# Optimization experiments

Measured on AMD Instinct MI355X. Metric: run time of the kernel, lower is better.

Reference implementation:

```python
import jax, jax.numpy as jnp
import numpy as np

B, T, D = 2, 2048, 1024
N, H = 16, 64  # num_heads, head_dim


def setup_inputs() -> dict:
    key = jax.random.key(0)
    ks = jax.random.split(key, 8)
    glorot = lambda k, shape, fan_in, fan_out: jax.random.uniform(
        k, shape, jnp.float32, -1.0, 1.0) * np.sqrt(6.0 / (fan_in + fan_out))
    return {
        "q": jax.random.normal(ks[0], (B, T, D), jnp.float32),
        "v": jax.random.normal(ks[1], (B, T, D), jnp.float32),
        "k": jax.random.normal(ks[2], (B, T, D), jnp.float32),
        "w_query": glorot(ks[3], (D, N, H), D, N * H),
        "b_query": jnp.zeros((N, 1, H), jnp.float32),
        "w_value": glorot(ks[4], (D, N, H), D, N * H),
        "b_value": jnp.zeros((N, 1, H), jnp.float32),
        "w_key": glorot(ks[5], (D, N, H), D, N * H),
        "b_key": jnp.zeros((N, 1, H), jnp.float32),
        "w_projection": glorot(ks[6], (N, D, H), N * H, D),
        "b_projection": jnp.zeros((1, D), jnp.float32),
    }


def reference(q, v, k, w_query, b_query, w_value, b_value, w_key, b_key,
              w_projection, b_projection):
    # QKV projections: [B,T,D] x [D,N,H] -> [B,N,T,H]
    query = jnp.einsum('btd,dnh->bnth', q, w_query) + b_query
    value = jnp.einsum('btd,dnh->bnth', v, w_value) + b_value
    key_p = jnp.einsum('btd,dnh->bnth', k, w_key) + b_key
    # Scaled dot-product attention, scores divided by sqrt(head_dim)
    scale = 1.0 / jnp.sqrt(jnp.asarray(H, query.dtype))
    scores = jnp.einsum('bnth,bnsh->bnts', query, key_p) * scale  # [B,N,T,T]
    weights = jax.nn.softmax(scores, axis=-1)
    attn = jnp.einsum('bnts,bnsh->bnth', weights, value)
    # Output projection: [B,N,T,H] x [N,D,H] -> [B,T,D]
    out = jnp.einsum('bnth,ndh->btd', attn, w_projection) + b_projection
    return out
```

## Files before the change

kernel.cpp:

```cpp
#include <hip/hip_runtime.h>
#include <hip/hip_bf16.h>
#include <cstdint>
#include <cstddef>


typedef __attribute__((ext_vector_type(8))) short short8;
typedef __attribute__((ext_vector_type(4))) float floatx4;
typedef __attribute__((ext_vector_type(8))) unsigned short ushort8;

#define EXP2F(x) __builtin_amdgcn_exp2f(x)

static __device__ __forceinline__ unsigned short f2bf(float f) {
    union { float f; unsigned int u; } v; v.f = f;
    unsigned int r = v.u + 0x7fffu + ((v.u >> 16) & 1u);
    return (unsigned short)(r >> 16);
}
static __device__ __forceinline__ unsigned int pk2bf(float lo, float hi) {
    __hip_bfloat162 t = __float22bfloat162_rn(make_float2(lo, hi));
    union { __hip_bfloat162 h; unsigned int u; } c; c.h = t;
    return c.u;
}
static __device__ __forceinline__ void gl_lds16(const unsigned short* g, unsigned short* l) {
    __builtin_amdgcn_global_load_lds(
        (const __attribute__((address_space(1))) unsigned int*)g,
        (__attribute__((address_space(3))) unsigned int*)l, 16, 0, 0);
}

__global__ __launch_bounds__(256) void mha_transpose_w(
    const float* __restrict__ wq, const float* __restrict__ wk, const float* __restrict__ wv,
    unsigned short* __restrict__ wqT, unsigned short* __restrict__ wkT, unsigned short* __restrict__ wvT)
{
    __shared__ float tile[32][33];
    const float* src; unsigned short* dst;
    int z = blockIdx.z;
    if (z == 0)      { src = wq; dst = wqT; }
    else if (z == 1) { src = wk; dst = wkT; }
    else             { src = wv; dst = wvT; }
    int n0 = blockIdx.x * 32, d0 = blockIdx.y * 32;
    int tx = threadIdx.x, ty = threadIdx.y;
    #pragma unroll
    for (int j = 0; j < 4; ++j)
        tile[ty + j * 8][tx] = src[(size_t)(d0 + ty + j * 8) * 1024 + n0 + tx];
    __syncthreads();
    #pragma unroll
    for (int j = 0; j < 4; ++j)
        dst[(size_t)(n0 + ty + j * 8) * 1024 + d0 + tx] = f2bf(tile[tx][ty + j * 8]);
}

__global__ __launch_bounds__(256) void mha_reorder_wp(
    const float* __restrict__ wp, unsigned short* __restrict__ wp2)
{
    int base = blockIdx.x * 1024 + threadIdx.x;
    #pragma unroll
    for (int i = 0; i < 4; ++i) {
        int idx = base + i * 256;
        int n = idx >> 16, d = (idx >> 6) & 1023, h = idx & 63;
        wp2[(size_t)d * 1024 + n * 64 + h] = f2bf(wp[idx]);
    }
}

__global__ __launch_bounds__(256) void prep_bf16_3(
    const float* __restrict__ x0, const float* __restrict__ x1, const float* __restrict__ x2,
    unsigned short* __restrict__ o0, unsigned short* __restrict__ o1, unsigned short* __restrict__ o2)
{
    int y = blockIdx.y;
    const float* x = y == 0 ? x0 : (y == 1 ? x1 : x2);
    unsigned short* o = y == 0 ? o0 : (y == 1 ? o1 : o2);
    size_t i = ((size_t)blockIdx.x * 256 + threadIdx.x) * 8;
    float4 a = *(const float4*)(x + i);
    float4 b = *(const float4*)(x + i + 4);
    uint4 pk;
    pk.x = pk2bf(a.x, a.y); pk.y = pk2bf(a.z, a.w);
    pk.z = pk2bf(b.x, b.y); pk.w = pk2bf(b.z, b.w);
    *(uint4*)(o + i) = pk;
}

__global__ __launch_bounds__(256) void gemm_qkv128(
    const unsigned short* __restrict__ A0, const unsigned short* __restrict__ A1,
    const unsigned short* __restrict__ A2,
    const unsigned short* __restrict__ W0, const unsigned short* __restrict__ W1,
    const unsigned short* __restrict__ W2,
    const float* __restrict__ b0, const float* __restrict__ b1, const float* __restrict__ b2,
    unsigned short* __restrict__ O0, unsigned short* __restrict__ O1, unsigned short* __restrict__ O2,
    float qscale, int matSel)
{
    __shared__ unsigned short As[128 * 32];
    __shared__ unsigned short Bs[128 * 32];
    int bm = blockIdx.x, by = blockIdx.y;
    int mat, nt;
    if (matSel < 0) { mat = by >> 3; nt = by & 7; } else { mat = matSel; nt = by; }
    const unsigned short* A  = mat == 0 ? A0 : (mat == 1 ? A1 : A2);
    const unsigned short* WT = mat == 0 ? W0 : (mat == 1 ? W1 : W2);
    const float* bias        = mat == 0 ? b0 : (mat == 1 ? b1 : b2);
    unsigned short* Out      = mat == 0 ? O0 : (mat == 1 ? O1 : O2);
    float scale = (mat == 0) ? qscale : 1.0f;
    int vmode = (mat == 2);

    int tid = threadIdx.x;
    int w = tid >> 6, lane = tid & 63, c15 = lane & 15, quad = lane >> 4;
    int wm = w >> 1, wn = w & 1;

    const unsigned short* gA[2]; unsigned short* lA[2];
    const unsigned short* gB[2]; unsigned short* lB[2];
    #pragma unroll
    for (int i = 0; i < 2; ++i) {
        int s = (w * 2 + i) * 64 + lane;
        gA[i] = A  + (size_t)(bm * 128 + (s >> 2)) * 1024 + (s & 3) * 8;
        lA[i] = &As[s * 8];
        gB[i] = WT + (size_t)(nt * 128 + (s >> 2)) * 1024 + (s & 3) * 8;
        lB[i] = &Bs[s * 8];
    }

    floatx4 acc[4][4];
    #pragma unroll
    for (int mi = 0; mi < 4; ++mi)
        #pragma unroll
        for (int ni = 0; ni < 4; ++ni) acc[mi][ni] = (floatx4){0.f, 0.f, 0.f, 0.f};

    for (int kt = 0; kt < 32; ++kt) {
        __syncthreads();
        #pragma unroll
        for (int i = 0; i < 2; ++i) { gl_lds16(gA[i] + kt * 32, lA[i]); gl_lds16(gB[i] + kt * 32, lB[i]); }
        __syncthreads();
        short8 af[4], bfr[4];
        #pragma unroll
        for (int mi = 0; mi < 4; ++mi)
            af[mi] = *(const short8*)&As[(wm * 64 + mi * 16 + c15) * 32 + quad * 8];
        #pragma unroll
        for (int ni = 0; ni < 4; ++ni)
            bfr[ni] = *(const short8*)&Bs[(wn * 64 + ni * 16 + c15) * 32 + quad * 8];
        #pragma unroll
        for (int mi = 0; mi < 4; ++mi)
            #pragma unroll
            for (int ni = 0; ni < 4; ++ni)
                acc[mi][ni] = __builtin_amdgcn_mfma_f32_16x16x32_bf16(af[mi], bfr[ni], acc[mi][ni], 0, 0, 0);
    }
    #pragma unroll
    for (int mi = 0; mi < 4; ++mi)
        #pragma unroll
        for (int ni = 0; ni < 4; ++ni)
            #pragma unroll
            for (int r = 0; r < 4; ++r) {
                int row = bm * 128 + wm * 64 + mi * 16 + quad * 4 + r;
                int col = nt * 128 + wn * 64 + ni * 16 + c15;
                float val = (acc[mi][ni][r] + bias[col]) * scale;
                int b = row >> 11, t = row & 2047, n = col >> 6, h = col & 63;
                if (vmode)
                    Out[((size_t)(b * 16 + n) * 64 + h) * 2048 + t] = f2bf(val);
                else
                    Out[((size_t)(b * 16 + n) * 2048 + t) * 64 + h] = f2bf(val);
            }
}

__global__ __launch_bounds__(256) void mha_flash3(
    const unsigned short* __restrict__ Qp, const unsigned short* __restrict__ Kp,
    const unsigned short* __restrict__ Vt, unsigned short* __restrict__ attnb)
{
    __shared__ unsigned short Ks[64 * 72];
    __shared__ unsigned short Vs[64 * 72];
    __shared__ unsigned short Pl[4][32 * 72];

    int bi = blockIdx.x;
    int xcd = bi & 7, j = bi >> 3;
    int bn = xcd * 4 + (j >> 4), qt = j & 15;
    int b = bn >> 4, n = bn & 15;
    int tid = threadIdx.x;
    int w = tid >> 6, lane = tid & 63, c15 = lane & 15, quad = lane >> 4;

    const unsigned short* Qb = Qp + (size_t)bn * 2048 * 64;
    const unsigned short* Kb = Kp + (size_t)bn * 2048 * 64;
    const unsigned short* Vb = Vt + (size_t)bn * 64 * 2048;

    int qbase = qt * 128 + w * 32;

    short8 bQ[2][2];
    #pragma unroll
    for (int tni = 0; tni < 2; ++tni)
        #pragma unroll
        for (int kc = 0; kc < 2; ++kc)
            bQ[tni][kc] = *(const short8*)(Qb + (size_t)(qbase + tni * 16 + c15) * 64 + kc * 32 + quad * 8);

    float l_i[2] = {0.f, 0.f};
    floatx4 o[2][4];
    #pragma unroll
    for (int i = 0; i < 2; ++i)
        #pragma unroll
        for (int j2 = 0; j2 < 4; ++j2) o[i][j2] = (floatx4){0.f, 0.f, 0.f, 0.f};

    unsigned short* Pw = &Pl[w][0];
    int srow = tid >> 3, scc = tid & 7;

    ushort8 kreg[2], vreg[2];
    #pragma unroll
    for (int i = 0; i < 2; ++i) {
        kreg[i] = *(const ushort8*)(Kb + (size_t)(srow + i * 32) * 64 + scc * 8);
        vreg[i] = *(const ushort8*)(Vb + (size_t)(srow + i * 32) * 2048 + scc * 8);
    }

    for (int it = 0; it < 32; ++it) {
        __syncthreads();
        #pragma unroll
        for (int i = 0; i < 2; ++i) {
            *(ushort8*)&Ks[(srow + i * 32) * 72 + scc * 8] = kreg[i];
            *(ushort8*)&Vs[(srow + i * 32) * 72 + scc * 8] = vreg[i];
        }
        if (it < 31) {
            int s1 = (it + 1) * 64;
            #pragma unroll
            for (int i = 0; i < 2; ++i) {
                kreg[i] = *(const ushort8*)(Kb + (size_t)(s1 + srow + i * 32) * 64 + scc * 8);
                vreg[i] = *(const ushort8*)(Vb + (size_t)(srow + i * 32) * 2048 + s1 + scc * 8);
            }
        }
        __syncthreads();

        floatx4 sc[4][2];
        #pragma unroll
        for (int smi = 0; smi < 4; ++smi) {
            short8 a0 = *(const short8*)&Ks[(smi * 16 + c15) * 72 + quad * 8];
            short8 a1 = *(const short8*)&Ks[(smi * 16 + c15) * 72 + 32 + quad * 8];
            #pragma unroll
            for (int tni = 0; tni < 2; ++tni) {
                floatx4 t = (floatx4){0.f, 0.f, 0.f, 0.f};
                t = __builtin_amdgcn_mfma_f32_16x16x32_bf16(a0, bQ[tni][0], t, 0, 0, 0);
                t = __builtin_amdgcn_mfma_f32_16x16x32_bf16(a1, bQ[tni][1], t, 0, 0, 0);
                sc[smi][tni] = t;
            }
        }
        #pragma unroll
        for (int tni = 0; tni < 2; ++tni) {
            float rs = 0.f;
            #pragma unroll
            for (int smi = 0; smi < 4; ++smi) {
                float p0 = EXP2F(sc[smi][tni][0]);
                float p1 = EXP2F(sc[smi][tni][1]);
                float p2 = EXP2F(sc[smi][tni][2]);
                float p3 = EXP2F(sc[smi][tni][3]);
                rs += (p0 + p1) + (p2 + p3);
                uint2 pw;
                pw.x = pk2bf(p0, p1);
                pw.y = pk2bf(p2, p3);
                *(uint2*)&Pw[(tni * 16 + c15) * 72 + smi * 16 + quad * 4] = pw;
            }
            l_i[tni] += rs;
        }
        short8 bv[4][2];
        #pragma unroll
        for (int hni = 0; hni < 4; ++hni)
            #pragma unroll
            for (int kc = 0; kc < 2; ++kc)
                bv[hni][kc] = *(const short8*)&Vs[(hni * 16 + c15) * 72 + kc * 32 + quad * 8];
        #pragma unroll
        for (int tmi = 0; tmi < 2; ++tmi) {
            short8 ap0 = *(const short8*)&Pw[(tmi * 16 + c15) * 72 + quad * 8];
            short8 ap1 = *(const short8*)&Pw[(tmi * 16 + c15) * 72 + 32 + quad * 8];
            #pragma unroll
            for (int hni = 0; hni < 4; ++hni) {
                o[tmi][hni] = __builtin_amdgcn_mfma_f32_16x16x32_bf16(ap0, bv[hni][0], o[tmi][hni], 0, 0, 0);
                o[tmi][hni] = __builtin_amdgcn_mfma_f32_16x16x32_bf16(ap1, bv[hni][1], o[tmi][hni], 0, 0, 0);
            }
        }
    }
    float lf[2];
    #pragma unroll
    for (int tmi = 0; tmi < 2; ++tmi) {
        float s = l_i[tmi];
        s += __shfl_xor(s, 16, 64);
        s += __shfl_xor(s, 32, 64);
        lf[tmi] = s;
    }
    #pragma unroll
    for (int tmi = 0; tmi < 2; ++tmi)
        #pragma unroll
        for (int r = 0; r < 4; ++r) {
            float linv = 1.0f / __shfl(lf[tmi], quad * 4 + r, 64);
            int t = qbase + tmi * 16 + quad * 4 + r;
            #pragma unroll
            for (int hni = 0; hni < 4; ++hni) {
                int col = n * 64 + hni * 16 + c15;
                attnb[(size_t)(b * 2048 + t) * 1024 + col] = f2bf(o[tmi][hni][r] * linv);
            }
        }
}

__global__ __launch_bounds__(256) void gemm_out64v2(
    const unsigned short* __restrict__ A, const unsigned short* __restrict__ BT,
    const float* __restrict__ bias, float* __restrict__ out)
{
    __shared__ unsigned short As[64 * 64];
    __shared__ unsigned short Bs[128 * 64];
    int bm = blockIdx.x, nt = blockIdx.y;
    int tid = threadIdx.x;
    int w = tid >> 6, lane = tid & 63, c15 = lane & 15, quad = lane >> 4;
    int wm = w >> 1, wn = w & 1;

    const unsigned short* gA[2]; unsigned short* lA[2];
    const unsigned short* gB[4]; unsigned short* lB[4];
    #pragma unroll
    for (int i = 0; i < 2; ++i) {
        int s = (w * 2 + i) * 64 + lane;
        int row = s >> 3, cl = (s & 7) ^ (row & 7);
        gA[i] = A + (size_t)(bm * 64 + row) * 1024 + cl * 8;
        lA[i] = &As[s * 8];
    }
    #pragma unroll
    for (int i = 0; i < 4; ++i) {
        int s = (w * 4 + i) * 64 + lane;
        int row = s >> 3, cl = (s & 7) ^ (row & 7);
        gB[i] = BT + (size_t)(nt * 128 + row) * 1024 + cl * 8;
        lB[i] = &Bs[s * 8];
    }

    floatx4 acc[2][4];
    #pragma unroll
    for (int mi = 0; mi < 2; ++mi)
        #pragma unroll
        for (int ni = 0; ni < 4; ++ni) acc[mi][ni] = (floatx4){0.f, 0.f, 0.f, 0.f};

    for (int kt = 0; kt < 16; ++kt) {
        __syncthreads();
        #pragma unroll
        for (int i = 0; i < 2; ++i) gl_lds16(gA[i] + kt * 64, lA[i]);
        #pragma unroll
        for (int i = 0; i < 4; ++i) gl_lds16(gB[i] + kt * 64, lB[i]);
        __syncthreads();
        #pragma unroll
        for (int kc = 0; kc < 2; ++kc) {
            short8 af[2], bfr[4];
            #pragma unroll
            for (int mi = 0; mi < 2; ++mi) {
                int row = wm * 32 + mi * 16 + c15;
                af[mi] = *(const short8*)&As[row * 64 + (((kc * 4 + quad) ^ (row & 7)) * 8)];
            }
            #pragma unroll
            for (int ni = 0; ni < 4; ++ni) {
                int row = wn * 64 + ni * 16 + c15;
                bfr[ni] = *(const short8*)&Bs[row * 64 + (((kc * 4 + quad) ^ (row & 7)) * 8)];
            }
            #pragma unroll
            for (int mi = 0; mi < 2; ++mi)
                #pragma unroll
                for (int ni = 0; ni < 4; ++ni)
                    acc[mi][ni] = __builtin_amdgcn_mfma_f32_16x16x32_bf16(af[mi], bfr[ni], acc[mi][ni], 0, 0, 0);
        }
    }
    #pragma unroll
    for (int mi = 0; mi < 2; ++mi)
        #pragma unroll
        for (int ni = 0; ni < 4; ++ni)
            #pragma unroll
            for (int r = 0; r < 4; ++r) {
                int row = bm * 64 + wm * 32 + mi * 16 + quad * 4 + r;
                int col = nt * 128 + wn * 64 + ni * 16 + c15;
                out[(size_t)row * 1024 + col] = acc[mi][ni][r] + bias[col];
            }
}

extern "C" void kernel_launch(void* const* d_in, const int* in_sizes, int n_in,
                              void* d_out, int out_size, void* d_ws, size_t ws_size,
                              hipStream_t stream)
{
    const float* q  = (const float*)d_in[0];
    const float* v  = (const float*)d_in[1];
    const float* k  = (const float*)d_in[2];
    const float* wq = (const float*)d_in[3];
    const float* bq = (const float*)d_in[4];
    const float* wv = (const float*)d_in[5];
    const float* bv = (const float*)d_in[6];
    const float* wk = (const float*)d_in[7];
    const float* bk = (const float*)d_in[8];
    const float* wp = (const float*)d_in[9];
    const float* bp = (const float*)d_in[10];
    float* out = (float*)d_out;

    char* ws = (char*)d_ws;
    unsigned short* wqT  = (unsigned short*)(ws + (size_t)0);
    unsigned short* wkT  = (unsigned short*)(ws + ((size_t)2  << 20));
    unsigned short* wvT  = (unsigned short*)(ws + ((size_t)4  << 20));
    unsigned short* wp2  = (unsigned short*)(ws + ((size_t)6  << 20));
    unsigned short* Qp   = (unsigned short*)(ws + ((size_t)8  << 20));
    unsigned short* Kp   = (unsigned short*)(ws + ((size_t)16 << 20));
    unsigned short* Vtp  = (unsigned short*)(ws + ((size_t)24 << 20));
    unsigned short* Xb   = (unsigned short*)(ws + ((size_t)32 << 20));
    unsigned short* attnb= (unsigned short*)(ws + ((size_t)32 << 20));

    const float qscale = 0.125f * 1.44269504088896f;

    hipLaunchKernelGGL(mha_transpose_w, dim3(32, 32, 3), dim3(32, 8), 0, stream,
                       wq, wk, wv, wqT, wkT, wvT);
    hipLaunchKernelGGL(mha_reorder_wp, dim3(1024), dim3(256), 0, stream, wp, wp2);

    if (ws_size >= ((size_t)64 << 20)) {
        unsigned short* qb = (unsigned short*)(ws + ((size_t)40 << 20));
        unsigned short* kb = (unsigned short*)(ws + ((size_t)48 << 20));
        unsigned short* vb = (unsigned short*)(ws + ((size_t)56 << 20));
        hipLaunchKernelGGL(prep_bf16_3, dim3(2048, 3), dim3(256), 0, stream, q, k, v, qb, kb, vb);
        hipLaunchKernelGGL(gemm_qkv128, dim3(32, 24), dim3(256), 0, stream,
                           qb, kb, vb, wqT, wkT, wvT, bq, bk, bv, Qp, Kp, Vtp, qscale, -1);
    } else {
        hipLaunchKernelGGL(prep_bf16_3, dim3(2048, 1), dim3(256), 0, stream, q, q, q, Xb, Xb, Xb);
        hipLaunchKernelGGL(gemm_qkv128, dim3(32, 8), dim3(256), 0, stream,
                           Xb, Xb, Xb, wqT, wkT, wvT, bq, bk, bv, Qp, Kp, Vtp, qscale, 0);
        hipLaunchKernelGGL(prep_bf16_3, dim3(2048, 1), dim3(256), 0, stream, k, k, k, Xb, Xb, Xb);
        hipLaunchKernelGGL(gemm_qkv128, dim3(32, 8), dim3(256), 0, stream,
                           Xb, Xb, Xb, wqT, wkT, wvT, bq, bk, bv, Qp, Kp, Vtp, qscale, 1);
        hipLaunchKernelGGL(prep_bf16_3, dim3(2048, 1), dim3(256), 0, stream, v, v, v, Xb, Xb, Xb);
        hipLaunchKernelGGL(gemm_qkv128, dim3(32, 8), dim3(256), 0, stream,
                           Xb, Xb, Xb, wqT, wkT, wvT, bq, bk, bv, Qp, Kp, Vtp, qscale, 2);
    }

    hipLaunchKernelGGL(mha_flash3, dim3(512), dim3(256), 0, stream, Qp, Kp, Vtp, attnb);
    hipLaunchKernelGGL(gemm_out64v2, dim3(64, 8), dim3(256), 0, stream, attnb, wp2, bp, out);
}
```

Baseline: 226.5 us.

## Separate V transpose kernel, XCD-aware block remapping, and MFMA priority hints

The fused QKV GEMM no longer writes V in transposed (scatter) layout. It writes V contiguously, and a new LDS-tiled transpose kernel then produces the transposed V used by attention. Both GEMM kernels remap block indices so blocks sharing weight or activation tiles land on the same XCD, aiming for better L2 reuse. The attention loop wraps its MFMA sections in s_setprio to favour matrix issue across waves. The cost is an extra kernel launch and an extra read/write pass over V.

```diff
diff --git a/kernel.cpp b/kernel.cpp
--- a/kernel.cpp
+++ b/kernel.cpp
@@ -75,6 +75,26 @@
     *(uint4*)(o + i) = pk;
 }
 
+__global__ __launch_bounds__(256) void mha_tr_v(
+    const unsigned short* __restrict__ Vp, unsigned short* __restrict__ Vt)
+{
+    __shared__ unsigned short tile[64][72];
+    int bn = blockIdx.x, tb = blockIdx.y;
+    int tid = threadIdx.x;
+    const unsigned short* src = Vp + ((size_t)bn * 2048 + tb * 64) * 64;
+    unsigned short* dst = Vt + (size_t)bn * 64 * 2048 + tb * 64;
+    int r = tid >> 2, cq = (tid & 3) * 16;
+    *(ushort8*)&tile[r][cq]     = *(const ushort8*)(src + r * 64 + cq);
+    *(ushort8*)&tile[r][cq + 8] = *(const ushort8*)(src + r * 64 + cq + 8);
+    __syncthreads();
+    int h = tid >> 2, t0 = (tid & 3) * 16;
+    ushort8 o0, o1;
+    #pragma unroll
+    for (int j = 0; j < 8; ++j) { o0[j] = tile[t0 + j][h]; o1[j] = tile[t0 + 8 + j][h]; }
+    *(ushort8*)(dst + (size_t)h * 2048 + t0)     = o0;
+    *(ushort8*)(dst + (size_t)h * 2048 + t0 + 8) = o1;
+}
+
 __global__ __launch_bounds__(256) void gemm_qkv128(
     const unsigned short* __restrict__ A0, const unsigned short* __restrict__ A1,
     const unsigned short* __restrict__ A2,
@@ -82,19 +102,24 @@
     const unsigned short* __restrict__ W2,
     const float* __restrict__ b0, const float* __restrict__ b1, const float* __restrict__ b2,
     unsigned short* __restrict__ O0, unsigned short* __restrict__ O1, unsigned short* __restrict__ O2,
-    float qscale, int matSel)
+    float qscale, int matSel, int scatterV)
 {
     __shared__ unsigned short As[128 * 32];
     __shared__ unsigned short Bs[128 * 32];
-    int bm = blockIdx.x, by = blockIdx.y;
-    int mat, nt;
-    if (matSel < 0) { mat = by >> 3; nt = by & 7; } else { mat = matSel; nt = by; }
+    int mat, nt, bm;
+    if (matSel < 0) {
+        int g = blockIdx.x + (blockIdx.y << 5);
+        int xcd = g & 7, s = g >> 3;
+        int grp = xcd * 3 + (s >> 5);
+        bm = s & 31;
+        mat = grp >> 3; nt = grp & 7;
+    } else { mat = matSel; nt = blockIdx.y; bm = blockIdx.x; }
     const unsigned short* A  = mat == 0 ? A0 : (mat == 1 ? A1 : A2);
     const unsigned short* WT = mat == 0 ? W0 : (mat == 1 ? W1 : W2);
     const float* bias        = mat == 0 ? b0 : (mat == 1 ? b1 : b2);
     unsigned short* Out      = mat == 0 ? O0 : (mat == 1 ? O1 : O2);
     float scale = (mat == 0) ? qscale : 1.0f;
-    int vmode = (mat == 2);
+    int vmode = (mat == 2) && scatterV;
 
     int tid = threadIdx.x;
     int w = tid >> 6, lane = tid & 63, c15 = lane & 15, quad = lane >> 4;
@@ -215,6 +240,7 @@
         __syncthreads();
 
         floatx4 sc[4][2];
+        __builtin_amdgcn_s_setprio(1);
         #pragma unroll
         for (int smi = 0; smi < 4; ++smi) {
             short8 a0 = *(const short8*)&Ks[(smi * 16 + c15) * 72 + quad * 8];
@@ -227,6 +253,7 @@
                 sc[smi][tni] = t;
             }
         }
+        __builtin_amdgcn_s_setprio(0);
         #pragma unroll
         for (int tni = 0; tni < 2; ++tni) {
             float rs = 0.f;
@@ -250,6 +277,7 @@
             #pragma unroll
             for (int kc = 0; kc < 2; ++kc)
                 bv[hni][kc] = *(const short8*)&Vs[(hni * 16 + c15) * 72 + kc * 32 + quad * 8];
+        __builtin_amdgcn_s_setprio(1);
         #pragma unroll
         for (int tmi = 0; tmi < 2; ++tmi) {
             short8 ap0 = *(const short8*)&Pw[(tmi * 16 + c15) * 72 + quad * 8];
@@ -260,6 +288,7 @@
                 o[tmi][hni] = __builtin_amdgcn_mfma_f32_16x16x32_bf16(ap1, bv[hni][1], o[tmi][hni], 0, 0, 0);
             }
         }
+        __builtin_amdgcn_s_setprio(0);
     }
     float lf[2];
     #pragma unroll
@@ -289,7 +318,8 @@
 {
     __shared__ unsigned short As[64 * 64];
     __shared__ unsigned short Bs[128 * 64];
-    int bm = blockIdx.x, nt = blockIdx.y;
+    int g = blockIdx.x + (blockIdx.y << 6);
+    int nt = g & 7, bm = g >> 3;
     int tid = threadIdx.x;
     int w = tid >> 6, lane = tid & 63, c15 = lane & 15, quad = lane >> 4;
     int wm = w >> 1, wn = w & 1;
@@ -394,19 +424,21 @@
         unsigned short* qb = (unsigned short*)(ws + ((size_t)40 << 20));
         unsigned short* kb = (unsigned short*)(ws + ((size_t)48 << 20));
         unsigned short* vb = (unsigned short*)(ws + ((size_t)56 << 20));
+        unsigned short* Vp = Xb;
         hipLaunchKernelGGL(prep_bf16_3, dim3(2048, 3), dim3(256), 0, stream, q, k, v, qb, kb, vb);
         hipLaunchKernelGGL(gemm_qkv128, dim3(32, 24), dim3(256), 0, stream,
-                           qb, kb, vb, wqT, wkT, wvT, bq, bk, bv, Qp, Kp, Vtp, qscale, -1);
+                           qb, kb, vb, wqT, wkT, wvT, bq, bk, bv, Qp, Kp, Vp, qscale, -1, 0);
+        hipLaunchKernelGGL(mha_tr_v, dim3(32, 32), dim3(256), 0, stream, Vp, Vtp);
     } else {
         hipLaunchKernelGGL(prep_bf16_3, dim3(2048, 1), dim3(256), 0, stream, q, q, q, Xb, Xb, Xb);
         hipLaunchKernelGGL(gemm_qkv128, dim3(32, 8), dim3(256), 0, stream,
-                           Xb, Xb, Xb, wqT, wkT, wvT, bq, bk, bv, Qp, Kp, Vtp, qscale, 0);
+                           Xb, Xb, Xb, wqT, wkT, wvT, bq, bk, bv, Qp, Kp, Vtp, qscale, 0, 1);
         hipLaunchKernelGGL(prep_bf16_3, dim3(2048, 1), dim3(256), 0, stream, k, k, k, Xb, Xb, Xb);
         hipLaunchKernelGGL(gemm_qkv128, dim3(32, 8), dim3(256), 0, stream,
-                           Xb, Xb, Xb, wqT, wkT, wvT, bq, bk, bv, Qp, Kp, Vtp, qscale, 1);
+                           Xb, Xb, Xb, wqT, wkT, wvT, bq, bk, bv, Qp, Kp, Vtp, qscale, 1, 1);
         hipLaunchKernelGGL(prep_bf16_3, dim3(2048, 1), dim3(256), 0, stream, v, v, v, Xb, Xb, Xb);
         hipLaunchKernelGGL(gemm_qkv128, dim3(32, 8), dim3(256), 0, stream,
-                           Xb, Xb, Xb, wqT, wkT, wvT, bq, bk, bv, Qp, Kp, Vtp, qscale, 2);
+                           Xb, Xb, Xb, wqT, wkT, wvT, bq, bk, bv, Qp, Kp, Vtp, qscale, 2, 1);
     }
 
     hipLaunchKernelGGL(mha_flash3, dim3(512), dim3(256), 0, stream, Qp, Kp, Vtp, attnb);
```

After: 231.8 us. 1.02x slower.
